# Kernel optimization log

Measured on AMD Instinct MI355X. Metric: run time of the kernel, lower is better.

## Reference

```python
import jax, jax.numpy as jnp
import numpy as np

B, T = 64, 2048
ENC_DIM, ATT_DIM, RNN_DIM, N_FILT, KSIZE, WIN = 512, 128, 1024, 32, 31, 32


def setup_inputs() -> dict:
    key = jax.random.key(0)
    ks = jax.random.split(key, 10)
    return {
        "attention_hidden_state": jax.random.normal(ks[0], (B, RNN_DIM), jnp.float32),
        "memory": jax.random.normal(ks[1], (B, T, ENC_DIM), jnp.float32),
        "processed_memory": jax.random.normal(ks[2], (B, T, ATT_DIM), jnp.float32),
        "attention_weights_cat": jax.random.uniform(ks[3], (B, 2, T), jnp.float32),
        "mask": jnp.zeros((B, T), jnp.bool_),
        "memory_lengths": jax.random.randint(ks[4], (B,), 0, T, jnp.int32),
        "current_pos": jax.random.uniform(ks[5], (B,), jnp.float32),
        "loc_conv_w": jax.random.normal(ks[6], (N_FILT, 2, KSIZE), jnp.float32) * 0.1,
        "loc_dense_w": jax.random.normal(ks[7], (ATT_DIM, N_FILT), jnp.float32) * 0.1,
        "query_w": jax.random.normal(ks[8], (ATT_DIM, RNN_DIM), jnp.float32) * 0.03,
        "v_w": jax.random.normal(ks[9], (1, ATT_DIM), jnp.float32) * 0.1,
        "pos_offset": jnp.zeros((1,), jnp.float32),
    }


def reference(attention_hidden_state, memory, processed_memory, attention_weights_cat,
              mask, memory_lengths, current_pos,
              loc_conv_w, loc_dense_w, query_w, v_w, pos_offset):
    Bn, Tn, _ = memory.shape
    pad = (KSIZE - 1) // 2
    # location conv: [B,2,T] -> [B,n_filters,T]
    conv = jax.lax.conv_general_dilated(
        attention_weights_cat, loc_conv_w, window_strides=(1,),
        padding=[(pad, pad)], dimension_numbers=("NCH", "OIH", "NCH"))
    # location dense + query projection + processed memory (fused add)
    processed = (jnp.einsum("bft,af->bta", conv, loc_dense_w)
                 + (attention_hidden_state @ query_w.T)[:, None, :]
                 + processed_memory)                      # [B,T,att_dim]
    alignment = jnp.tanh(processed) @ v_w[0]              # [B,T]
    # dynamic windowed mask around current_pos
    cp = current_pos + pos_offset[0]
    max_end = (memory_lengths - 1 - WIN).astype(cp.dtype)
    cp = jnp.minimum(jnp.maximum(cp, jnp.float32(WIN)), max_end)
    mask_start = jnp.round(jnp.maximum(cp - WIN, 0.0))
    mask_end = mask_start + 2 * WIN
    pos = jnp.arange(Tn, dtype=cp.dtype)
    pos_mask = (pos[None, :] >= mask_start[:, None]) & (pos[None, :] <= mask_end[:, None])
    full_mask = mask | ~pos_mask
    alignment = jnp.where(full_mask, jnp.float32(-1e9), alignment)
    attention_weights = jax.nn.softmax(alignment, axis=1)  # [B,T]
    attention_context = jnp.einsum("bt,btd->bd", attention_weights, memory)  # [B,enc_dim]
    new_pos = attention_weights @ jnp.arange(Tn, dtype=attention_weights.dtype)  # [B]
    return attention_context, attention_weights, new_pos
```

## Files before the change

kernel.cpp:

```cpp
#include <hip/hip_runtime.h>
#include <math.h>

#define Bn 64
#define Tn 2048
#define ENC 512
#define ATT 128
#define RNN 1024
#define NF 32
#define KS 31
#define WINR 32
#define WSZ 65
#define HALO 95
#define WPAD 68


__global__ __launch_bounds__(512)
void attn_stage1(
    const float* __restrict__ hidden,
    const float* __restrict__ pmem,
    const float* __restrict__ cat,
    const unsigned char* __restrict__ mask,
    const int*  __restrict__ mlen,
    const float* __restrict__ cpos,
    const float* __restrict__ convw,
    const float* __restrict__ densew,
    const float* __restrict__ qw,
    const float* __restrict__ vw,
    const float* __restrict__ posoff,
    float* __restrict__ out,
    float* __restrict__ ws_w,
    int*   __restrict__ ws_s)
{
    __shared__ float s_hidden[RNN];
    __shared__ float s_part[512];
    __shared__ float s_qproj[ATT];
    __shared__ float s_ldw[ATT * 33];
    __shared__ float s_cw[NF * 2 * KS];
    __shared__ float s_cat[2 * HALO];
    __shared__ float s_conv[WSZ * NF];
    __shared__ float s_pm[WSZ * ATT];
    __shared__ float s_align[WSZ];
    __shared__ float s_w[WSZ];

    const int b = blockIdx.x;
    const int tid = threadIdx.x;

    float cp = cpos[b] + posoff[0];
    float mend = (float)(mlen[b] - 1 - WINR);
    cp = fminf(fmaxf(cp, (float)WINR), mend);
    int s = (int)rintf(fmaxf(cp - (float)WINR, 0.0f));
    if (s < 0) s = 0;
    if (s > Tn - WSZ) s = Tn - WSZ;

    for (int i = tid; i < RNN / 4; i += 512)
        ((float4*)s_hidden)[i] = ((const float4*)(hidden + (size_t)b * RNN))[i];
    {
        const float4* pmw = (const float4*)(pmem + ((size_t)b * Tn + s) * ATT);
        for (int i = tid; i < WSZ * ATT / 4; i += 512)
            ((float4*)s_pm)[i] = pmw[i];
    }
    for (int i = tid; i < ATT * NF; i += 512) {
        int a = i >> 5, f = i & 31;
        s_ldw[a * 33 + f] = densew[i];
    }
    for (int i = tid; i < NF * 2 * KS; i += 512) s_cw[i] = convw[i];
    for (int i = tid; i < 2 * HALO; i += 512) {
        int c = i / HALO, j = i - c * HALO;
        int t = s - (KS - 1) / 2 + j;
        float v = 0.0f;
        if (t >= 0 && t < Tn) v = cat[((size_t)b * 2 + c) * Tn + t];
        s_cat[c * HALO + j] = v;
    }
    __syncthreads();

    {
        int a = tid & 127, q = tid >> 7;
        const float4* q4 = (const float4*)(qw + (size_t)a * RNN + q * 256);
        const float4* h4 = (const float4*)(s_hidden + q * 256);
        float acc = 0.0f;
#pragma unroll 8
        for (int i = 0; i < 64; i++) {
            float4 x = q4[i], h = h4[i];
            acc += x.x * h.x + x.y * h.y + x.z * h.z + x.w * h.w;
        }
        s_part[tid] = acc;
    }
    __syncthreads();
    if (tid < ATT)
        s_qproj[tid] = s_part[tid] + s_part[tid + 128] + s_part[tid + 256] + s_part[tid + 384];

    for (int i = tid; i < WSZ * NF; i += 512) {
        int j = i >> 5, f = i & 31;
        const float* w0 = s_cw + f * 2 * KS;
        const float* c0 = s_cat + j;
        const float* c1 = s_cat + HALO + j;
        float acc = 0.0f;
#pragma unroll
        for (int k = 0; k < KS; k++) acc += c0[k] * w0[k] + c1[k] * w0[KS + k];
        s_conv[i] = acc;
    }
    __syncthreads();

    const int lane = tid & 63;
    const int wv = tid >> 6;
    const float va0 = vw[lane];
    const float va1 = vw[lane + 64];
    for (int j = wv; j < WSZ; j += 8) {
        const float* pmr = s_pm + j * ATT;
        const float* cv = s_conv + j * NF;
        const float* l0 = s_ldw + lane * 33;
        const float* l1 = s_ldw + (lane + 64) * 33;
        float x0 = s_qproj[lane] + pmr[lane];
        float x1 = s_qproj[lane + 64] + pmr[lane + 64];
#pragma unroll
        for (int f = 0; f < NF; f++) {
            float c = cv[f];
            x0 += c * l0[f];
            x1 += c * l1[f];
        }
        float val = tanhf(x0) * va0 + tanhf(x1) * va1;
        for (int off = 32; off > 0; off >>= 1) val += __shfl_down(val, off);
        if (lane == 0) {
            bool mk = mask[(size_t)b * Tn + s + j] != 0;
            s_align[j] = mk ? -1e9f : val;
        }
    }
    __syncthreads();

    if (tid < WSZ) {
        float m = -1e30f;
        for (int j = 0; j < WSZ; j++) m = fmaxf(m, s_align[j]);
        float sum = 0.0f;
        for (int j = 0; j < WSZ; j++) sum += expf(s_align[j] - m);
        s_w[tid] = expf(s_align[tid] - m) / sum;
    }
    __syncthreads();

    if (tid == 0) {
        float np = 0.0f;
        for (int j = 0; j < WSZ; j++) np += s_w[j] * (float)(s + j);
        out[(size_t)Bn * ENC + (size_t)Bn * Tn + b] = np;
        ws_s[b] = s;
    }
    if (tid < WSZ) ws_w[b * WPAD + tid] = s_w[tid];

    {
        float4* wout = (float4*)(out + (size_t)Bn * ENC + (size_t)b * Tn);
        for (int i = tid; i < Tn / 4; i += 512) {
            float4 v;
            float* vv = (float*)&v;
#pragma unroll
            for (int q = 0; q < 4; q++) {
                int j = i * 4 + q - s;
                vv[q] = (j >= 0 && j < WSZ) ? s_w[j] : 0.0f;
            }
            wout[i] = v;
        }
    }
}

__global__ __launch_bounds__(128)
void attn_ctx(
    const float* __restrict__ memory,
    const float* __restrict__ ws_w,
    const int*  __restrict__ ws_s,
    float* __restrict__ out)
{
    __shared__ float s_w[WSZ];
    __shared__ int s_sv;
    const int b = blockIdx.x >> 2;
    const int r = blockIdx.x & 3;
    const int tid = threadIdx.x;
    if (tid < WSZ) s_w[tid] = ws_w[b * WPAD + tid];
    if (tid == 0) s_sv = ws_s[b];
    __syncthreads();
    const int s = s_sv;
    const float* mb = memory + (size_t)b * Tn * ENC + r * 128 + tid;
    float acc = 0.0f;
#pragma unroll 5
    for (int j = 0; j < WSZ; j++)
        acc += s_w[j] * mb[(size_t)(s + j) * ENC];
    out[(size_t)b * ENC + r * 128 + tid] = acc;
}

extern "C" void kernel_launch(void* const* d_in, const int* in_sizes, int n_in,
                              void* d_out, int out_size, void* d_ws, size_t ws_size,
                              hipStream_t stream) {
    float* ws_w = (float*)d_ws;
    int*   ws_s = (int*)((char*)d_ws + Bn * WPAD * 4);

    attn_stage1<<<Bn, 512, 0, stream>>>(
        (const float*)d_in[0],
        (const float*)d_in[2],
        (const float*)d_in[3],
        (const unsigned char*)d_in[4],
        (const int*)d_in[5],
        (const float*)d_in[6],
        (const float*)d_in[7],
        (const float*)d_in[8],
        (const float*)d_in[9],
        (const float*)d_in[10],
        (const float*)d_in[11],
        (float*)d_out, ws_w, ws_s);

    attn_ctx<<<Bn * 4, 128, 0, stream>>>(
        (const float*)d_in[1],
        ws_w, ws_s, (float*)d_out);
}
```

Before: 381.2 us.

## Fuse context reduction into stage-1 kernel and prefetch memory window into registers

Merges the separate context kernel into the score/softmax kernel, removing a second launch and the workspace round-trip for weights and window start. Each thread issues its windowed memory loads (33 float2 per thread) at the start, before the projection, conv and softmax work, so the memory latency overlaps that computation. A two-way shared reduction then produces the context. The cost is high register pressure (66 extra floats per thread at 512 threads) and only 64 blocks doing the memory read, where the old context kernel used 256.

After: 376.2 us. No clear change (-1.3%).

```diff
diff --git a/kernel.cpp b/kernel.cpp
--- a/kernel.cpp
+++ b/kernel.cpp
@@ -11,12 +11,12 @@
 #define WINR 32
 #define WSZ 65
 #define HALO 95
-#define WPAD 68
-
-
-__global__ __launch_bounds__(512)
-void attn_stage1(
+#define NTH 512
+
+__global__ __launch_bounds__(NTH)
+void attn_fused(
     const float* __restrict__ hidden,
+    const float* __restrict__ memory,
     const float* __restrict__ pmem,
     const float* __restrict__ cat,
     const unsigned char* __restrict__ mask,
@@ -27,20 +27,20 @@
     const float* __restrict__ qw,
     const float* __restrict__ vw,
     const float* __restrict__ posoff,
-    float* __restrict__ out,
-    float* __restrict__ ws_w,
-    int*   __restrict__ ws_s)
+    float* __restrict__ out)
 {
     __shared__ float s_hidden[RNN];
-    __shared__ float s_part[512];
+    __shared__ float s_part[NTH];
     __shared__ float s_qproj[ATT];
     __shared__ float s_ldw[ATT * 33];
     __shared__ float s_cw[NF * 2 * KS];
     __shared__ float s_cat[2 * HALO];
     __shared__ float s_conv[WSZ * NF];
     __shared__ float s_pm[WSZ * ATT];
+    __shared__ unsigned char s_mk[WSZ];
     __shared__ float s_align[WSZ];
     __shared__ float s_w[WSZ];
+    __shared__ float2 s_red[2 * (ENC / 2)];
 
     const int b = blockIdx.x;
     const int tid = threadIdx.x;
@@ -52,24 +52,36 @@
     if (s < 0) s = 0;
     if (s > Tn - WSZ) s = Tn - WSZ;
 
-    for (int i = tid; i < RNN / 4; i += 512)
+    for (int i = tid; i < RNN / 4; i += NTH)
         ((float4*)s_hidden)[i] = ((const float4*)(hidden + (size_t)b * RNN))[i];
     {
         const float4* pmw = (const float4*)(pmem + ((size_t)b * Tn + s) * ATT);
-        for (int i = tid; i < WSZ * ATT / 4; i += 512)
+        for (int i = tid; i < WSZ * ATT / 4; i += NTH)
             ((float4*)s_pm)[i] = pmw[i];
     }
-    for (int i = tid; i < ATT * NF; i += 512) {
+    for (int i = tid; i < ATT * NF; i += NTH) {
         int a = i >> 5, f = i & 31;
         s_ldw[a * 33 + f] = densew[i];
     }
-    for (int i = tid; i < NF * 2 * KS; i += 512) s_cw[i] = convw[i];
-    for (int i = tid; i < 2 * HALO; i += 512) {
-        int c = i / HALO, j = i - c * HALO;
+    for (int i = tid; i < NF * 2 * KS; i += NTH) s_cw[i] = convw[i];
+    for (int i = tid; i < 2 * HALO; i += NTH) {
+        int cch = i / HALO, j = i - cch * HALO;
         int t = s - (KS - 1) / 2 + j;
         float v = 0.0f;
-        if (t >= 0 && t < Tn) v = cat[((size_t)b * 2 + c) * Tn + t];
-        s_cat[c * HALO + j] = v;
+        if (t >= 0 && t < Tn) v = cat[((size_t)b * 2 + cch) * Tn + t];
+        s_cat[cch * HALO + j] = v;
+    }
+    if (tid < WSZ) s_mk[tid] = mask[(size_t)b * Tn + s + tid];
+
+    const int c = tid & 255;
+    const int g = tid >> 8;
+    float2 v[33];
+    const float2* m2 = (const float2*)(memory + (size_t)b * Tn * ENC)
+                       + (size_t)(s + g) * (ENC / 2) + c;
+#pragma unroll
+    for (int i = 0; i < 33; i++) {
+        int j = g + 2 * i;
+        if (j < WSZ) v[i] = m2[(size_t)(2 * i) * (ENC / 2)];
     }
     __syncthreads();
 
@@ -89,7 +101,7 @@
     if (tid < ATT)
         s_qproj[tid] = s_part[tid] + s_part[tid + 128] + s_part[tid + 256] + s_part[tid + 384];
 
-    for (int i = tid; i < WSZ * NF; i += 512) {
+    for (int i = tid; i < WSZ * NF; i += NTH) {
         int j = i >> 5, f = i & 31;
         const float* w0 = s_cw + f * 2 * KS;
         const float* c0 = s_cat + j;
@@ -114,16 +126,13 @@
         float x1 = s_qproj[lane + 64] + pmr[lane + 64];
 #pragma unroll
         for (int f = 0; f < NF; f++) {
-            float c = cv[f];
-            x0 += c * l0[f];
-            x1 += c * l1[f];
+            float cc = cv[f];
+            x0 += cc * l0[f];
+            x1 += cc * l1[f];
         }
         float val = tanhf(x0) * va0 + tanhf(x1) * va1;
         for (int off = 32; off > 0; off >>= 1) val += __shfl_down(val, off);
-        if (lane == 0) {
-            bool mk = mask[(size_t)b * Tn + s + j] != 0;
-            s_align[j] = mk ? -1e9f : val;
-        }
+        if (lane == 0) s_align[j] = s_mk[j] ? -1e9f : val;
     }
     __syncthreads();
 
@@ -140,57 +149,49 @@
         float np = 0.0f;
         for (int j = 0; j < WSZ; j++) np += s_w[j] * (float)(s + j);
         out[(size_t)Bn * ENC + (size_t)Bn * Tn + b] = np;
-        ws_s[b] = s;
-    }
-    if (tid < WSZ) ws_w[b * WPAD + tid] = s_w[tid];
+    }
 
     {
         float4* wout = (float4*)(out + (size_t)Bn * ENC + (size_t)b * Tn);
-        for (int i = tid; i < Tn / 4; i += 512) {
-            float4 v;
-            float* vv = (float*)&v;
+        for (int i = tid; i < Tn / 4; i += NTH) {
+            float4 vv;
+            float* vp = (float*)&vv;
 #pragma unroll
             for (int q = 0; q < 4; q++) {
                 int j = i * 4 + q - s;
-                vv[q] = (j >= 0 && j < WSZ) ? s_w[j] : 0.0f;
+                vp[q] = (j >= 0 && j < WSZ) ? s_w[j] : 0.0f;
             }
-            wout[i] = v;
-        }
-    }
-}
-
-__global__ __launch_bounds__(128)
-void attn_ctx(
-    const float* __restrict__ memory,
-    const float* __restrict__ ws_w,
-    const int*  __restrict__ ws_s,
-    float* __restrict__ out)
-{
-    __shared__ float s_w[WSZ];
-    __shared__ int s_sv;
-    const int b = blockIdx.x >> 2;
-    const int r = blockIdx.x & 3;
-    const int tid = threadIdx.x;
-    if (tid < WSZ) s_w[tid] = ws_w[b * WPAD + tid];
-    if (tid == 0) s_sv = ws_s[b];
-    __syncthreads();
-    const int s = s_sv;
-    const float* mb = memory + (size_t)b * Tn * ENC + r * 128 + tid;
-    float acc = 0.0f;
-#pragma unroll 5
-    for (int j = 0; j < WSZ; j++)
-        acc += s_w[j] * mb[(size_t)(s + j) * ENC];
-    out[(size_t)b * ENC + r * 128 + tid] = acc;
+            wout[i] = vv;
+        }
+    }
+
+    {
+        float2 acc = make_float2(0.0f, 0.0f);
+#pragma unroll
+        for (int i = 0; i < 33; i++) {
+            int j = g + 2 * i;
+            if (j < WSZ) {
+                float wj = s_w[j];
+                acc.x += wj * v[i].x;
+                acc.y += wj * v[i].y;
+            }
+        }
+        s_red[g * (ENC / 2) + c] = acc;
+    }
+    __syncthreads();
+    if (tid < ENC / 2) {
+        float2 a = s_red[tid], bb = s_red[(ENC / 2) + tid];
+        float2 r = make_float2(a.x + bb.x, a.y + bb.y);
+        ((float2*)out)[(size_t)b * (ENC / 2) + tid] = r;
+    }
 }
 
 extern "C" void kernel_launch(void* const* d_in, const int* in_sizes, int n_in,
                               void* d_out, int out_size, void* d_ws, size_t ws_size,
                               hipStream_t stream) {
-    float* ws_w = (float*)d_ws;
-    int*   ws_s = (int*)((char*)d_ws + Bn * WPAD * 4);
-
-    attn_stage1<<<Bn, 512, 0, stream>>>(
+    attn_fused<<<Bn, NTH, 0, stream>>>(
         (const float*)d_in[0],
+        (const float*)d_in[1],
         (const float*)d_in[2],
         (const float*)d_in[3],
         (const unsigned char*)d_in[4],
@@ -201,9 +202,5 @@
         (const float*)d_in[9],
         (const float*)d_in[10],
         (const float*)d_in[11],
-        (float*)d_out, ws_w, ws_s);
-
-    attn_ctx<<<Bn * 4, 128, 0, stream>>>(
-        (const float*)d_in[1],
-        ws_w, ws_s, (float*)d_out);
+        (float*)d_out);
 }
```
